# Kernel tuning notes

Hardware: AMD Instinct MI355X
Metric: run time of the kernel (lower is better)

The kernel has to match this reference:

```python
import jax, jax.numpy as jnp
import numpy as np

NQ = 10000   # num_q
N = 512      # n (seq len)
D = 512      # d (model dim)
H = 8        # attention heads
LW = 64      # local window
B = 16       # batch


def _mha(q, k, v, wi, bi, wo, bo, nh, mask=None):
    # torch nn.MultiheadAttention math (eval mode, dropout off), batch-first inputs
    Bq, S, d = q.shape
    hd = d // nh
    wq, wk, wv = jnp.split(wi, 3, axis=0)
    bq, bk, bv = jnp.split(bi, 3)

    def proj(x, w, b):
        y = x @ w.T + b
        return y.reshape(x.shape[0], x.shape[1], nh, hd).transpose(0, 2, 1, 3)  # [B,h,S,hd]

    Q = proj(q, wq, bq)
    K = proj(k, wk, bk)
    V = proj(v, wv, bv)
    s = jnp.einsum('bhqe,bhke->bhqk', Q, K) / jnp.sqrt(jnp.asarray(hd, q.dtype))
    if mask is not None:
        s = jnp.where(mask[None, None], -jnp.inf, s)
    w = jax.nn.softmax(s, axis=-1)
    o = jnp.einsum('bhqk,bhke->bhqe', w, V).transpose(0, 2, 1, 3).reshape(Bq, S, d)
    return o @ wo.T + bo, w.mean(axis=1)  # avg over heads like torch default


def _ln(x, g, b):
    m = x.mean(-1, keepdims=True)
    v = ((x - m) ** 2).mean(-1, keepdims=True)
    return (x - m) / jnp.sqrt(v + 1e-5) * g + b


def setup_inputs() -> dict:
    key = jax.random.key(0)
    ks = iter(jax.random.split(key, 40))
    f = lambda *sh: jax.random.normal(next(ks), sh, jnp.float32) * 0.02
    inp = {
        'q': jax.random.randint(next(ks), (B, N), 0, NQ, jnp.int32),
        'r': jax.random.randint(next(ks), (B, N), 0, 2, jnp.int32),
        'qry': jax.random.randint(next(ks), (B, N), 0, NQ, jnp.int32),
        'M_emb': f(2 * NQ, D),
        'E_emb': f(NQ, D),
        'P': f(N, D),
    }
    for nm in ['base', 'local', 'glob', 'cross']:
        inp[nm + '_in_w'] = f(3 * D, D)
        inp[nm + '_in_b'] = jnp.zeros((3 * D,), jnp.float32)
        inp[nm + '_out_w'] = f(D, D)
        inp[nm + '_out_b'] = jnp.zeros((D,), jnp.float32)
    inp['ln1_g'] = jnp.ones((D,), jnp.float32)
    inp['ln1_b'] = jnp.zeros((D,), jnp.float32)
    inp['w1'] = f(D, D)
    inp['b1'] = jnp.zeros((D,), jnp.float32)
    inp['w2'] = f(D, D)
    inp['b2'] = jnp.zeros((D,), jnp.float32)
    inp['ln2_g'] = jnp.ones((D,), jnp.float32)
    inp['ln2_b'] = jnp.zeros((D,), jnp.float32)
    inp['pred_w'] = f(1, D)
    inp['pred_b'] = jnp.zeros((1,), jnp.float32)
    return inp


def reference(q, r, qry, M_emb, E_emb, P,
              base_in_w, base_in_b, base_out_w, base_out_b,
              local_in_w, local_in_b, local_out_w, local_out_b,
              glob_in_w, glob_in_b, glob_out_w, glob_out_b,
              cross_in_w, cross_in_b, cross_out_w, cross_out_b,
              ln1_g, ln1_b, w1, b1, w2, b2, ln2_g, ln2_b, pred_w, pred_b):
    x = q + NQ * r
    M = M_emb[x] + P[None]          # [B,N,D], positional added as in torch code
    E = E_emb[qry]                  # [B,N,D]
    cm = jnp.triu(jnp.ones((N, N), bool), 1)

    S_base, attn_w = _mha(E, M, M, base_in_w, base_in_b, base_out_w, base_out_b, H, cm)
    S_base = _ln(S_base + M + E, ln1_g, ln1_b)

    lm = jnp.triu(jnp.ones((LW, LW), bool), 1)
    s_loc_in = S_base[:, -LW:, :]
    S_loc, _ = _mha(s_loc_in, s_loc_in, s_loc_in, local_in_w, local_in_b, local_out_w, local_out_b, H, lm)
    S_local = jnp.concatenate([jnp.zeros((S_base.shape[0], N - LW, D), S_base.dtype), S_loc], axis=1)

    S_global, _ = _mha(S_base, S_base, S_base, glob_in_w, glob_in_b, glob_out_w, glob_out_b, H, cm)
    S_cross, _ = _mha(S_base, S_local, S_local, cross_in_w, cross_in_b, cross_out_w, cross_out_b, H, None)

    S = S_base + S_local + S_global + S_cross
    F = jax.nn.relu(S @ w1.T + b1) @ w2.T + b2
    F = _ln(F + S, ln2_g, ln2_b)
    p = jax.nn.sigmoid(F @ pred_w.T + pred_b)[..., 0]   # [B,N]
    return p, attn_w
```

## Files before the change

kernel.cpp:

```cpp
#include <hip/hip_runtime.h>
#include <hip/hip_bf16.h>

#define D_MODEL 512
#define NHEAD 8
#define NSEQ 512
#define BATCH 16
#define LWIN 64
#define S2C 0.18033688f
#define L2E 1.44269504f

typedef short s16x8 __attribute__((ext_vector_type(8)));
typedef float f32x4 __attribute__((ext_vector_type(4)));

__device__ inline unsigned short f2bf(float f) {
    unsigned int u = __float_as_uint(f);
    u = (u + 0x7fffu + ((u >> 16) & 1u)) >> 16;
    return (unsigned short)u;
}
__device__ inline int sw4(int r) { return (r + (r >> 2)) & 3; }

#define GLD16(g, l) __builtin_amdgcn_global_load_lds( \
    (const __attribute__((address_space(1))) void*)(g), \
    (__attribute__((address_space(3))) void*)(l), 16, 0, 0)

struct WP { const float* p[10]; };

__global__ __launch_bounds__(256) void front_kernel(
    WP wp, unsigned short* __restrict__ Wb, unsigned short* __restrict__ Z,
    const int* __restrict__ q, const int* __restrict__ r, const int* __restrict__ qry,
    const float* __restrict__ M_emb, const float* __restrict__ E_emb,
    const float* __restrict__ P, float* __restrict__ Mf, float* __restrict__ Ef,
    unsigned short* __restrict__ Mb, unsigned short* __restrict__ Eb)
{
    const int blk = blockIdx.x, tid = threadIdx.x;
    if (blk < 4608) {
        const long e = ((long)blk * 256 + tid) * 4;
        const float* src; long loc;
        if (e < 3145728) { int rg = (int)(e / 786432); src = wp.p[rg]; loc = e - (long)rg * 786432; }
        else { long j = e - 3145728; int rg = (int)(j >> 18); src = wp.p[4 + rg]; loc = j - ((long)rg << 18); }
        float4 v = *(const float4*)(src + loc);
        ushort4 o; o.x = f2bf(v.x); o.y = f2bf(v.y); o.z = f2bf(v.z); o.w = f2bf(v.w);
        *(ushort4*)(Wb + e) = o;
    } else if (blk < 6656) {
        const long i = ((long)(blk - 4608) * 256 + tid) * 8;
        *(uint4*)(Z + i) = make_uint4(0u, 0u, 0u, 0u);
    } else {
        const int t = (blk - 6656) * 2 + (tid >> 7);
        const int i = tid & 127;
        const int n = t & (NSEQ - 1);
        const int x = q[t] + 10000 * r[t];
        const int e = qry[t];
        float4 a = ((const float4*)(M_emb + (long)x * D_MODEL))[i];
        float4 p4 = ((const float4*)(P + (long)n * D_MODEL))[i];
        float4 ev = ((const float4*)(E_emb + (long)e * D_MODEL))[i];
        float4 mv = make_float4(a.x + p4.x, a.y + p4.y, a.z + p4.z, a.w + p4.w);
        ((float4*)(Mf + (long)t * D_MODEL))[i] = mv;
        ((float4*)(Ef + (long)t * D_MODEL))[i] = ev;
        ushort4 mb; mb.x = f2bf(mv.x); mb.y = f2bf(mv.y); mb.z = f2bf(mv.z); mb.w = f2bf(mv.w);
        ushort4 eb; eb.x = f2bf(ev.x); eb.y = f2bf(ev.y); eb.z = f2bf(ev.z); eb.w = f2bf(ev.w);
        *(ushort4*)(Mb + (long)t * D_MODEL + i * 4) = mb;
        *(ushort4*)(Eb + (long)t * D_MODEL + i * 4) = eb;
    }
}

struct GArgs {
    const unsigned short* A; const unsigned short* A2; int nsplit;
    const unsigned short* W; const float* bias;
    unsigned short* Cb; int ldcb; int crem;
    float* Cf; int ldcf;
    const float* r1; const float* r2; const float* tl;
    int relu; int arem;
};

__global__ __launch_bounds__(256) void gemm_bf16(GArgs g0, GArgs g1, int msplit)
{
    __shared__ __align__(16) unsigned short Sh[6144];
    unsigned short* As = Sh;
    unsigned short* Ws = Sh + 4096;
    float* Shf = (float*)Sh;

    int m0 = blockIdx.y * 128;
    const GArgs& G = (m0 < msplit) ? g0 : g1;
    if (m0 >= msplit) m0 -= msplit;

    const int tid = threadIdx.x, lane = tid & 63, wid = tid >> 6;
    const int n0 = blockIdx.x * 64;
    const int lm = lane & 15;
    const int lq = lane >> 4;
    const unsigned short* Asel = (n0 >= G.nsplit) ? G.A2 : G.A;

    const int rlane = lane >> 2, clane = lane & 3;
    const int lr0 = wid * 16 + rlane;
    const int lr1 = 64 + lr0;
    int rgA0 = m0 + lr0, rgA1 = m0 + lr1;
    if (G.arem) {
        rgA0 = ((rgA0 >> 6) << 9) + (NSEQ - LWIN) + (rgA0 & 63);
        rgA1 = ((rgA1 >> 6) << 9) + (NSEQ - LWIN) + (rgA1 & 63);
    }
    const unsigned short* pA0 = Asel + (long)rgA0 * 512 + ((clane ^ sw4(lr0)) << 3);
    const unsigned short* pA1 = Asel + (long)rgA1 * 512 + ((clane ^ sw4(lr1)) << 3);
    const unsigned short* pW0 = G.W + (long)(n0 + lr0) * 512 + ((clane ^ sw4(lr0)) << 3);
    unsigned short* lA0 = As + (wid * 16) * 32;
    unsigned short* lA1 = As + (64 + wid * 16) * 32;
    unsigned short* lW0 = Ws + (wid * 16) * 32;

    f32x4 acc[2][4];
    #pragma unroll
    for (int i = 0; i < 2; ++i)
        #pragma unroll
        for (int j = 0; j < 4; ++j) acc[i][j] = (f32x4){0.f, 0.f, 0.f, 0.f};

    for (int k0 = 0; k0 < 512; k0 += 32) {
        __syncthreads();
        GLD16(pA0 + k0, lA0);
        GLD16(pA1 + k0, lA1);
        GLD16(pW0 + k0, lW0);
        __syncthreads();

        s16x8 af[2], wf[4];
        #pragma unroll
        for (int i = 0; i < 2; ++i) {
            const int ra = wid * 32 + i * 16 + lm;
            af[i] = *(const s16x8*)&As[ra * 32 + ((lq ^ sw4(ra)) << 3)];
        }
        #pragma unroll
        for (int j = 0; j < 4; ++j) {
            const int rw = j * 16 + lm;
            wf[j] = *(const s16x8*)&Ws[rw * 32 + ((lq ^ sw4(rw)) << 3)];
        }
        #pragma unroll
        for (int i = 0; i < 2; ++i)
            #pragma unroll
            for (int j = 0; j < 4; ++j)
                acc[i][j] = __builtin_amdgcn_mfma_f32_16x16x32_bf16(af[i], wf[j], acc[i][j], 0, 0, 0);
    }

    const int fr = lane & 15;
    const int q4 = (lane >> 4) * 4;
    for (int qtr = 0; qtr < 4; ++qtr) {
        __syncthreads();
        if (wid == qtr) {
            #pragma unroll
            for (int j = 0; j < 4; ++j) {
                const int lcol = j * 16 + fr;
                const float bv = G.bias[n0 + lcol];
                #pragma unroll
                for (int i = 0; i < 2; ++i) {
                    #pragma unroll
                    for (int rg = 0; rg < 4; ++rg) {
                        float v = acc[i][j][rg] + bv;
                        if (G.relu) v = fmaxf(v, 0.f);
                        Shf[(i * 16 + q4 + rg) * 68 + lcol] = v;
                    }
                }
            }
        }
        __syncthreads();
        #pragma unroll
        for (int it = 0; it < 2; ++it) {
            const int flat = it * 256 + tid;
            const int rowq = flat >> 4, k4 = flat & 15;
            const int grow = m0 + qtr * 32 + rowq;
            const int gcol = n0 + k4 * 4;
            float4 f = *(const float4*)&Shf[rowq * 68 + k4 * 4];
            if (G.r1) {
                float4 a = *(const float4*)(G.r1 + (long)grow * 512 + gcol);
                f.x += a.x; f.y += a.y; f.z += a.z; f.w += a.w;
            }
            if (G.r2) {
                float4 b = *(const float4*)(G.r2 + (long)grow * 512 + gcol);
                f.x += b.x; f.y += b.y; f.z += b.z; f.w += b.w;
            }
            if (G.tl) {
                const int n = grow & 511;
                if (n >= NSEQ - LWIN) {
                    float4 c = *(const float4*)(G.tl + ((long)(grow >> 9) * 64 + (n - (NSEQ - LWIN))) * 512 + gcol);
                    f.x += c.x; f.y += c.y; f.z += c.z; f.w += c.w;
                }
            }
            if (G.Cf) *(float4*)(G.Cf + (long)grow * G.ldcf + gcol) = f;
            if (G.Cb) {
                const int crow = G.crem ? (((grow >> 6) << 9) + (NSEQ - LWIN) + (grow & 63)) : grow;
                ushort4 u; u.x = f2bf(f.x); u.y = f2bf(f.y); u.z = f2bf(f.z); u.w = f2bf(f.w);
                *(ushort4*)(G.Cb + (long)crow * G.ldcb + gcol) = u;
            }
        }
    }
}

struct FArgs {
    const unsigned short* Q; const unsigned short* K; const unsigned short* V;
    unsigned short* O; float* stats; int Nq, Nkv, ldq, ldkv, causal;
};

__global__ __launch_bounds__(256) void flash_mfma(FArgs f0, FArgs f1, int xsplit)
{
    __shared__ __align__(16) unsigned short Ks[64 * 72];
    __shared__ __align__(16) unsigned short Pl[64 * 72];
    __shared__ __align__(16) unsigned int   Vt[64 * 36];

    const FArgs& F = ((int)blockIdx.x < xsplit) ? f0 : f1;
    const int bx = ((int)blockIdx.x < xsplit) ? blockIdx.x : (blockIdx.x - xsplit);

    const int tid = threadIdx.x, lane = tid & 63, w = tid >> 6;
    const int lm = lane & 15, lq = lane >> 4;
    const int h = blockIdx.y, b = blockIdx.z;
    const int Nq = F.Nq, Nkv = F.Nkv, ldq = F.ldq, ldkv = F.ldkv, causal = F.causal;
    const int nqt = Nq >> 6;
    const int qa = bx, qb = nqt - 1 - qa;
    const bool single = (qa == qb);

    s16x8 aqA0, aqA1, aqB0, aqB1;
    {
        const unsigned short* qp = F.Q + ((long)b * Nq + qb * 64 + w * 16 + lm) * ldq + h * 64 + lq * 8;
        aqB0 = *(const s16x8*)qp; aqB1 = *(const s16x8*)(qp + 32);
    }
    if (!single) {
        const unsigned short* qp = F.Q + ((long)b * Nq + qa * 64 + w * 16 + lm) * ldq + h * 64 + lq * 8;
        aqA0 = *(const s16x8*)qp; aqA1 = *(const s16x8*)(qp + 32);
    }

    float mA = -INFINITY, lA = 0.f, mB = -INFINITY, lB = 0.f;
    f32x4 oA[4], oB[4];
    #pragma unroll
    for (int t = 0; t < 4; ++t) { oA[t] = (f32x4){0.f,0.f,0.f,0.f}; oB[t] = (f32x4){0.f,0.f,0.f,0.f}; }

    const int nkt = causal ? (qb + 1) : (Nkv >> 6);
    const int skey = tid >> 3, sd = (tid & 7) * 8;

    s16x8 kr0, kr1; uint4 vr0, vr1;
    {
        const long kb = ((long)b * Nkv) * ldkv + h * 64;
        kr0 = *(const s16x8*)(F.K + kb + (long)skey * ldkv + sd);
        kr1 = *(const s16x8*)(F.K + kb + (long)(skey + 32) * ldkv + sd);
        const unsigned short* vp = F.V + ((long)b * Nkv + 2 * skey) * ldkv + h * 64 + sd;
        vr0 = *(const uint4*)vp; vr1 = *(const uint4*)(vp + ldkv);
    }

    auto process = [&](s16x8 a0, s16x8 a1, float& m, float& l, f32x4* oacc, bool diag) {
        f32x4 sc[4];
        #pragma unroll
        for (int t = 0; t < 4; ++t) sc[t] = (f32x4){0.f,0.f,0.f,0.f};
        #pragma unroll
        for (int t = 0; t < 4; ++t) {
            s16x8 k0 = *(const s16x8*)&Ks[(t * 16 + lm) * 72 + lq * 8];
            s16x8 k1 = *(const s16x8*)&Ks[(t * 16 + lm) * 72 + lq * 8 + 32];
            sc[t] = __builtin_amdgcn_mfma_f32_16x16x32_bf16(k0, a0, sc[t], 0, 0, 0);
            sc[t] = __builtin_amdgcn_mfma_f32_16x16x32_bf16(k1, a1, sc[t], 0, 0, 0);
        }
        if (diag) {
            #pragma unroll
            for (int t = 0; t < 4; ++t)
                #pragma unroll
                for (int r = 0; r < 4; ++r)
                    if (t * 16 + lq * 4 + r > w * 16 + lm) sc[t][r] = -INFINITY;
        }
        float mt = sc[0][0];
        #pragma unroll
        for (int t = 0; t < 4; ++t)
            #pragma unroll
            for (int r = 0; r < 4; ++r) mt = fmaxf(mt, sc[t][r]);
        mt = fmaxf(mt, __shfl_xor(mt, 16));
        mt = fmaxf(mt, __shfl_xor(mt, 32));
        const float mn = fmaxf(m, mt);
        const float al = exp2f((m - mn) * S2C);
        float rs = 0.f;
        #pragma unroll
        for (int t = 0; t < 4; ++t)
            #pragma unroll
            for (int r = 0; r < 4; ++r) {
                float p = exp2f((sc[t][r] - mn) * S2C);
                sc[t][r] = p; rs += p;
            }
        rs += __shfl_xor(rs, 16);
        rs += __shfl_xor(rs, 32);
        m = mn; l = l * al + rs;
        #pragma unroll
        for (int t = 0; t < 4; ++t) oacc[t] *= al;
        #pragma unroll
        for (int t = 0; t < 4; ++t) {
            ushort4 u;
            u.x = f2bf(sc[t][0]); u.y = f2bf(sc[t][1]);
            u.z = f2bf(sc[t][2]); u.w = f2bf(sc[t][3]);
            *(ushort4*)&Pl[(w * 16 + lm) * 72 + t * 16 + lq * 4] = u;
        }
        #pragma unroll
        for (int ks = 0; ks < 2; ++ks) {
            s16x8 bp = *(const s16x8*)&Pl[(w * 16 + lm) * 72 + ks * 32 + lq * 8];
            #pragma unroll
            for (int t = 0; t < 4; ++t) {
                const int row = t * 16 + lm;
                const int pg = ((lq >> 1) + 2 * ks) ^ ((row >> 3) & 3);
                s16x8 av = *(const s16x8*)((const unsigned short*)Vt + row * 72 + pg * 16 + (lq & 1) * 8);
                oacc[t] = __builtin_amdgcn_mfma_f32_16x16x32_bf16(av, bp, oacc[t], 0, 0, 0);
            }
        }
    };

    for (int kt = 0; kt < nkt; ++kt) {
        __syncthreads();
        *(s16x8*)&Ks[skey * 72 + sd] = kr0;
        *(s16x8*)&Ks[(skey + 32) * 72 + sd] = kr1;
        {
            unsigned pw[8];
            pw[0] = (vr0.x & 0xffffu) | (vr1.x << 16);
            pw[1] = (vr0.x >> 16)     | (vr1.x & 0xffff0000u);
            pw[2] = (vr0.y & 0xffffu) | (vr1.y << 16);
            pw[3] = (vr0.y >> 16)     | (vr1.y & 0xffff0000u);
            pw[4] = (vr0.z & 0xffffu) | (vr1.z << 16);
            pw[5] = (vr0.z >> 16)     | (vr1.z & 0xffff0000u);
            pw[6] = (vr0.w & 0xffffu) | (vr1.w << 16);
            pw[7] = (vr0.w >> 16)     | (vr1.w & 0xffff0000u);
            #pragma unroll
            for (int j = 0; j < 8; ++j) {
                const int row = sd + j;
                const int col = (((skey >> 3) ^ ((row >> 3) & 3)) << 3) | (skey & 7);
                Vt[row * 36 + col] = pw[j];
            }
        }
        __syncthreads();
        if (kt + 1 < nkt) {
            const long kb = ((long)b * Nkv + (kt + 1) * 64) * ldkv + h * 64;
            kr0 = *(const s16x8*)(F.K + kb + (long)skey * ldkv + sd);
            kr1 = *(const s16x8*)(F.K + kb + (long)(skey + 32) * ldkv + sd);
            const unsigned short* vp = F.V + ((long)b * Nkv + (kt + 1) * 64 + 2 * skey) * ldkv + h * 64 + sd;
            vr0 = *(const uint4*)vp; vr1 = *(const uint4*)(vp + ldkv);
        }
        process(aqB0, aqB1, mB, lB, oB, causal && (kt == qb));
        if (!single && (!causal || kt <= qa))
            process(aqA0, aqA1, mA, lA, oA, causal && (kt == qa));
    }

    {
        const float inv = 1.0f / lB;
        const long orow = ((long)b * Nq + qb * 64 + w * 16 + lm) * D_MODEL + h * 64;
        #pragma unroll
        for (int t = 0; t < 4; ++t) {
            ushort4 u;
            u.x = f2bf(oB[t][0] * inv); u.y = f2bf(oB[t][1] * inv);
            u.z = f2bf(oB[t][2] * inv); u.w = f2bf(oB[t][3] * inv);
            *(ushort4*)(F.O + orow + t * 16 + lq * 4) = u;
        }
    }
    if (!single) {
        const float inv = 1.0f / lA;
        const long orow = ((long)b * Nq + qa * 64 + w * 16 + lm) * D_MODEL + h * 64;
        #pragma unroll
        for (int t = 0; t < 4; ++t) {
            ushort4 u;
            u.x = f2bf(oA[t][0] * inv); u.y = f2bf(oA[t][1] * inv);
            u.z = f2bf(oA[t][2] * inv); u.w = f2bf(oA[t][3] * inv);
            *(ushort4*)(F.O + orow + t * 16 + lq * 4) = u;
        }
    }
    if (F.stats && lq == 0) {
        long idx = (((long)b * NHEAD + h) * Nq + qb * 64 + w * 16 + lm) * 2;
        F.stats[idx] = mB * 0.125f; F.stats[idx + 1] = lB;
        if (!single) {
            idx = (((long)b * NHEAD + h) * Nq + qa * 64 + w * 16 + lm) * 2;
            F.stats[idx] = mA * 0.125f; F.stats[idx + 1] = lA;
        }
    }
}

__global__ __launch_bounds__(256) void attn_w_kernel(
    const unsigned short* __restrict__ Q, const unsigned short* __restrict__ K,
    const float* __restrict__ stats, float* __restrict__ AW, int ldq, int ldk)
{
    const int kt = blockIdx.x, qt = blockIdx.y, b = blockIdx.z;
    const int tid = threadIdx.x;
    if (kt > qt) {
        const int tx = tid & 15, ty = tid >> 4;
        #pragma unroll
        for (int i = 0; i < 4; ++i)
            *(float4*)(AW + ((long)b * NSEQ + qt * 64 + ty * 4 + i) * NSEQ + kt * 64 + tx * 4)
                = make_float4(0.f, 0.f, 0.f, 0.f);
        return;
    }
    __shared__ __align__(16) unsigned short Ks[64 * 72];
    const int lane = tid & 63, w = tid >> 6;
    const int lm = lane & 15, lq = lane >> 4;
    const int skey = tid >> 3, sd = (tid & 7) * 8;
    const long qrow = (long)b * NSEQ + qt * 64 + w * 16 + lm;

    f32x4 aw[4];
    #pragma unroll
    for (int t = 0; t < 4; ++t) aw[t] = (f32x4){0.f,0.f,0.f,0.f};

    for (int h = 0; h < NHEAD; ++h) {
        __syncthreads();
        {
            const long kb = ((long)b * NSEQ + kt * 64) * ldk + h * 64;
            *(s16x8*)&Ks[skey * 72 + sd] = *(const s16x8*)(K + kb + (long)skey * ldk + sd);
            *(s16x8*)&Ks[(skey + 32) * 72 + sd] = *(const s16x8*)(K + kb + (long)(skey + 32) * ldk + sd);
        }
        __syncthreads();
        s16x8 a0, a1;
        {
            const unsigned short* qp = Q + qrow * ldq + h * 64 + lq * 8;
            a0 = *(const s16x8*)qp; a1 = *(const s16x8*)(qp + 32);
        }
        f32x4 sc[4];
        #pragma unroll
        for (int t = 0; t < 4; ++t) sc[t] = (f32x4){0.f,0.f,0.f,0.f};
        #pragma unroll
        for (int t = 0; t < 4; ++t) {
            s16x8 k0 = *(const s16x8*)&Ks[(t * 16 + lm) * 72 + lq * 8];
            s16x8 k1 = *(const s16x8*)&Ks[(t * 16 + lm) * 72 + lq * 8 + 32];
            sc[t] = __builtin_amdgcn_mfma_f32_16x16x32_bf16(k0, a0, sc[t], 0, 0, 0);
            sc[t] = __builtin_amdgcn_mfma_f32_16x16x32_bf16(k1, a1, sc[t], 0, 0, 0);
        }
        float2 ml = *(const float2*)(stats + (((long)b * NHEAD + h) * NSEQ + qt * 64 + w * 16 + lm) * 2);
        const float mb2 = ml.x * L2E;
        const float sca = 0.125f / ml.y;
        #pragma unroll
        for (int t = 0; t < 4; ++t)
            #pragma unroll
            for (int r = 0; r < 4; ++r) {
                const bool masked = (kt == qt) && (t * 16 + lq * 4 + r > w * 16 + lm);
                if (!masked) aw[t][r] += exp2f(sc[t][r] * S2C - mb2) * sca;
            }
    }
    #pragma unroll
    for (int t = 0; t < 4; ++t)
        *(float4*)(AW + qrow * NSEQ + kt * 64 + t * 16 + lq * 4) = float4{aw[t][0], aw[t][1], aw[t][2], aw[t][3]};
}

__global__ __launch_bounds__(256) void ln_kernel(
    const float* __restrict__ X, const float* __restrict__ R1,
    const float* __restrict__ R2, const float* __restrict__ g,
    const float* __restrict__ bb, float* __restrict__ outf,
    unsigned short* __restrict__ outb,
    const float* __restrict__ pw, const float* __restrict__ pb,
    float* __restrict__ outp)
{
    const long row = blockIdx.x;
    const int tid = threadIdx.x;
    __shared__ float red[256];
    const long base = row * D_MODEL;
    float v0 = X[base + tid], v1 = X[base + tid + 256];
    if (R1) { v0 += R1[base + tid]; v1 += R1[base + tid + 256]; }
    if (R2) { v0 += R2[base + tid]; v1 += R2[base + tid + 256]; }
    red[tid] = v0 + v1; __syncthreads();
    for (int s = 128; s > 0; s >>= 1) {
        if (tid < s) red[tid] += red[tid + s];
        __syncthreads();
    }
    const float mean = red[0] * (1.f / 512.f);
    __syncthreads();
    const float d0 = v0 - mean, d1 = v1 - mean;
    red[tid] = d0 * d0 + d1 * d1; __syncthreads();
    for (int s = 128; s > 0; s >>= 1) {
        if (tid < s) red[tid] += red[tid + s];
        __syncthreads();
    }
    const float rstd = rsqrtf(red[0] * (1.f / 512.f) + 1e-5f);
    const float y0 = d0 * rstd * g[tid] + bb[tid];
    const float y1 = d1 * rstd * g[tid + 256] + bb[tid + 256];
    if (pw) {
        float s = y0 * pw[tid] + y1 * pw[tid + 256];
        __syncthreads();
        red[tid] = s; __syncthreads();
        for (int st = 128; st > 0; st >>= 1) {
            if (tid < st) red[tid] += red[tid + st];
            __syncthreads();
        }
        if (tid == 0) outp[row] = 1.f / (1.f + __expf(-(red[0] + pb[0])));
        return;
    }
    if (outf) { outf[base + tid] = y0; outf[base + tid + 256] = y1; }
    if (outb) { outb[base + tid] = f2bf(y0); outb[base + tid + 256] = f2bf(y1); }
}

extern "C" void kernel_launch(void* const* d_in, const int* in_sizes, int n_in,
                              void* d_out, int out_size, void* d_ws, size_t ws_size,
                              hipStream_t stream)
{
    const int*   q          = (const int*)d_in[0];
    const int*   r          = (const int*)d_in[1];
    const int*   qry        = (const int*)d_in[2];
    const float* M_emb      = (const float*)d_in[3];
    const float* E_emb      = (const float*)d_in[4];
    const float* P          = (const float*)d_in[5];
    const float* base_in_w  = (const float*)d_in[6];
    const float* base_in_b  = (const float*)d_in[7];
    const float* base_out_w = (const float*)d_in[8];
    const float* base_out_b = (const float*)d_in[9];
    const float* local_in_w = (const float*)d_in[10];
    const float* local_in_b = (const float*)d_in[11];
    const float* local_out_w= (const float*)d_in[12];
    const float* local_out_b= (const float*)d_in[13];
    const float* glob_in_w  = (const float*)d_in[14];
    const float* glob_in_b  = (const float*)d_in[15];
    const float* glob_out_w = (const float*)d_in[16];
    const float* glob_out_b = (const float*)d_in[17];
    const float* cross_in_w = (const float*)d_in[18];
    const float* cross_in_b = (const float*)d_in[19];
    const float* cross_out_w= (const float*)d_in[20];
    const float* cross_out_b= (const float*)d_in[21];
    const float* ln1_g      = (const float*)d_in[22];
    const float* ln1_b      = (const float*)d_in[23];
    const float* w1         = (const float*)d_in[24];
    const float* b1         = (const float*)d_in[25];
    const float* w2         = (const float*)d_in[26];
    const float* b2         = (const float*)d_in[27];
    const float* ln2_g      = (const float*)d_in[28];
    const float* ln2_b      = (const float*)d_in[29];
    const float* pred_w     = (const float*)d_in[30];
    const float* pred_b     = (const float*)d_in[31];
    float* out = (float*)d_out;

    char* p = (char*)d_ws;
    unsigned short* Wb = (unsigned short*)p; p += 4718592L * 2;
    unsigned short* B[11];
    for (int i = 0; i < 11; ++i) { B[i] = (unsigned short*)p; p += 8388608L; }
    unsigned short* Obl   = (unsigned short*)p; p += 1048576L;
    unsigned short* QKV3L = (unsigned short*)p; p += 3145728L;
    float* R[4];
    for (int i = 0; i < 4; ++i) { R[i] = (float*)p; p += 16777216L; }
    float* Tloc  = (float*)p; p += 2097152L;
    float* stats = (float*)p; p += 524288L;

    unsigned short* Mb = B[0];
    unsigned short* Eb = B[1];      unsigned short* Oc_b = B[1];
    unsigned short* QKVb = B[2];
    unsigned short* Sb_b = B[2];
    unsigned short* Ob  = B[5];
    unsigned short* Sbase_b  = B[6];
    unsigned short* Slocal_b = B[7];
    unsigned short* QKV3 = B[8];
    unsigned short* H1_b = B[8];
    float* Mf = R[0];
    float* Ef = R[1];       float* Sbuf_f   = R[1];
    float* Tb_f = R[2];     float* Sglobal_f= R[2];
    float* Sbase_f = R[3];  float* Fpre_f   = R[3];

    const long oBin = 0, oLin = 786432, oGin = 1572864, oCin = 2359296;
    const long oBout = 3145728, oLout = 3407872, oGout = 3670016, oCout = 3932160;
    const long oW1 = 4194304, oW2 = 4456448;
    const int BIG = 1 << 30;
    const unsigned short* NUS = nullptr;
    const float* NF = nullptr;

    auto GA = [](const unsigned short* A, const unsigned short* A2, int nsplit,
                 const unsigned short* W, const float* bias,
                 unsigned short* Cb, int ldcb, int crem, float* Cf, int ldcf,
                 const float* r1, const float* r2, const float* tl, int relu, int arem) {
        GArgs g; g.A = A; g.A2 = A2; g.nsplit = nsplit; g.W = W; g.bias = bias;
        g.Cb = Cb; g.ldcb = ldcb; g.crem = crem; g.Cf = Cf; g.ldcf = ldcf;
        g.r1 = r1; g.r2 = r2; g.tl = tl; g.relu = relu; g.arem = arem; return g;
    };
    auto FA = [](const unsigned short* Q, const unsigned short* K, const unsigned short* V,
                 unsigned short* O, float* stats, int Nq, int Nkv, int ldq, int ldkv, int causal) {
        FArgs f; f.Q = Q; f.K = K; f.V = V; f.O = O; f.stats = stats;
        f.Nq = Nq; f.Nkv = Nkv; f.ldq = ldq; f.ldkv = ldkv; f.causal = causal; return f;
    };

    WP wp; wp.p[0] = base_in_w; wp.p[1] = local_in_w; wp.p[2] = glob_in_w; wp.p[3] = cross_in_w;
    wp.p[4] = base_out_w; wp.p[5] = local_out_w; wp.p[6] = glob_out_w; wp.p[7] = cross_out_w;
    wp.p[8] = w1; wp.p[9] = w2;
    front_kernel<<<10752, 256, 0, stream>>>(wp, Wb, Slocal_b, q, r, qry, M_emb, E_emb, P, Mf, Ef, Mb, Eb);

    GArgs gBase = GA(Eb, Mb, 512, Wb + oBin, base_in_b, QKVb, 1536, 0, nullptr, 0, NF, NF, NF, 0, 0);
    gemm_bf16<<<dim3(24, 64), 256, 0, stream>>>(gBase, gBase, BIG);
    FArgs fBase = FA(QKVb, QKVb + 512, QKVb + 1024, Ob, stats, 512, 512, 1536, 1536, 1);
    flash_mfma<<<dim3(4, NHEAD, BATCH), 256, 0, stream>>>(fBase, fBase, BIG);
    attn_w_kernel<<<dim3(8, 8, BATCH), 256, 0, stream>>>(QKVb, QKVb + 512, stats, out + 8192, 1536, 1536);
    GArgs gBo = GA(Ob, NUS, BIG, Wb + oBout, base_out_b, nullptr, 0, 0, Tb_f, 512, Mf, Ef, NF, 0, 0);
    gemm_bf16<<<dim3(8, 64), 256, 0, stream>>>(gBo, gBo, BIG);
    ln_kernel<<<8192, 256, 0, stream>>>(Tb_f, NF, NF, ln1_g, ln1_b, Sbase_f, Sbase_b, NF, NF, nullptr);

    GArgs gGin = GA(Sbase_b, NUS, BIG, Wb + oGin, glob_in_b, QKV3, 1536, 0, nullptr, 0, NF, NF, NF, 0, 0);
    GArgs gLin = GA(Sbase_b, NUS, BIG, Wb + oLin, local_in_b, QKV3L, 1536, 0, nullptr, 0, NF, NF, NF, 0, 1);
    gemm_bf16<<<dim3(24, 72), 256, 0, stream>>>(gGin, gLin, 8192);

    FArgs fGlob = FA(QKV3, QKV3 + 512, QKV3 + 1024, Ob, nullptr, 512, 512, 1536, 1536, 1);
    FArgs fLoc  = FA(QKV3L, QKV3L + 512, QKV3L + 1024, Obl, nullptr, 64, 64, 1536, 1536, 1);
    flash_mfma<<<dim3(5, NHEAD, BATCH), 256, 0, stream>>>(fGlob, fLoc, 4);

    GArgs gGo = GA(Ob, NUS, BIG, Wb + oGout, glob_out_b, nullptr, 0, 0, Sglobal_f, 512, NF, NF, NF, 0, 0);
    GArgs gLo = GA(Obl, NUS, BIG, Wb + oLout, local_out_b, Slocal_b, 512, 1, Tloc, 512, NF, NF, NF, 0, 0);
    gemm_bf16<<<dim3(8, 72), 256, 0, stream>>>(gGo, gLo, 8192);

    GArgs gCin = GA(Sbase_b, Slocal_b, 512, Wb + oCin, cross_in_b, QKVb, 1536, 0, nullptr, 0, NF, NF, NF, 0, 0);
    gemm_bf16<<<dim3(24, 64), 256, 0, stream>>>(gCin, gCin, BIG);
    FArgs fCross = FA(QKVb, QKVb + 512, QKVb + 1024, Oc_b, nullptr, 512, 512, 1536, 1536, 0);
    flash_mfma<<<dim3(4, NHEAD, BATCH), 256, 0, stream>>>(fCross, fCross, BIG);
    GArgs gCo = GA(Oc_b, NUS, BIG, Wb + oCout, cross_out_b, Sb_b, 512, 0, Sbuf_f, 512,
                   Sbase_f, Sglobal_f, Tloc, 0, 0);
    gemm_bf16<<<dim3(8, 64), 256, 0, stream>>>(gCo, gCo, BIG);

    GArgs gF1 = GA(Sb_b, NUS, BIG, Wb + oW1, b1, H1_b, 512, 0, nullptr, 0, NF, NF, NF, 1, 0);
    gemm_bf16<<<dim3(8, 64), 256, 0, stream>>>(gF1, gF1, BIG);
    GArgs gF2 = GA(H1_b, NUS, BIG, Wb + oW2, b2, nullptr, 0, 0, Fpre_f, 512, Sbuf_f, NF, NF, 0, 0);
    gemm_bf16<<<dim3(8, 64), 256, 0, stream>>>(gF2, gF2, BIG);
    ln_kernel<<<8192, 256, 0, stream>>>(Fpre_f, NF, NF, ln2_g, ln2_b,
        nullptr, nullptr, pred_w, pred_b, out);
}
```

Before: 497.0 us.

## Store fp32 intermediates as bf16 and fuse attention-weight kernel into QKV GEMM launch

Every fp32 intermediate (embeddings, residual sums, pre-LN outputs, global/local branches) is now stored and read as bf16, which removes the fp32 copies and roughly halves the memory traffic of the epilogues and layernorms. The standalone attention-weight kernel is merged into the global/local QKV GEMM launch as extra blocks, so the two run concurrently and one launch is saved. The cost is lower precision on the residual paths and layernorm inputs, which could move outputs closer to the tolerance limit.

```diff
diff --git a/kernel.cpp b/kernel.cpp
--- a/kernel.cpp
+++ b/kernel.cpp
@@ -17,6 +17,11 @@
     u = (u + 0x7fffu + ((u >> 16) & 1u)) >> 16;
     return (unsigned short)u;
 }
+__device__ inline float4 bfl4(const unsigned short* p) {
+    uint2 u = *(const uint2*)p;
+    return make_float4(__uint_as_float(u.x << 16), __uint_as_float(u.x & 0xffff0000u),
+                       __uint_as_float(u.y << 16), __uint_as_float(u.y & 0xffff0000u));
+}
 __device__ inline int sw4(int r) { return (r + (r >> 2)) & 3; }
 
 #define GLD16(g, l) __builtin_amdgcn_global_load_lds( \
@@ -29,7 +34,7 @@
     WP wp, unsigned short* __restrict__ Wb, unsigned short* __restrict__ Z,
     const int* __restrict__ q, const int* __restrict__ r, const int* __restrict__ qry,
     const float* __restrict__ M_emb, const float* __restrict__ E_emb,
-    const float* __restrict__ P, float* __restrict__ Mf, float* __restrict__ Ef,
+    const float* __restrict__ P,
     unsigned short* __restrict__ Mb, unsigned short* __restrict__ Eb)
 {
     const int blk = blockIdx.x, tid = threadIdx.x;
@@ -54,8 +59,6 @@
         float4 p4 = ((const float4*)(P + (long)n * D_MODEL))[i];
         float4 ev = ((const float4*)(E_emb + (long)e * D_MODEL))[i];
         float4 mv = make_float4(a.x + p4.x, a.y + p4.y, a.z + p4.z, a.w + p4.w);
-        ((float4*)(Mf + (long)t * D_MODEL))[i] = mv;
-        ((float4*)(Ef + (long)t * D_MODEL))[i] = ev;
         ushort4 mb; mb.x = f2bf(mv.x); mb.y = f2bf(mv.y); mb.z = f2bf(mv.z); mb.w = f2bf(mv.w);
         ushort4 eb; eb.x = f2bf(ev.x); eb.y = f2bf(ev.y); eb.z = f2bf(ev.z); eb.w = f2bf(ev.w);
         *(ushort4*)(Mb + (long)t * D_MODEL + i * 4) = mb;
@@ -67,24 +70,19 @@
     const unsigned short* A; const unsigned short* A2; int nsplit;
     const unsigned short* W; const float* bias;
     unsigned short* Cb; int ldcb; int crem;
-    float* Cf; int ldcf;
-    const float* r1; const float* r2; const float* tl;
+    unsigned short* Cb2; int ldcb2;
+    const unsigned short* r1; const unsigned short* r2; const unsigned short* tl;
     int relu; int arem;
 };
 
-__global__ __launch_bounds__(256) void gemm_bf16(GArgs g0, GArgs g1, int msplit)
-{
-    __shared__ __align__(16) unsigned short Sh[6144];
+__device__ __forceinline__ void gemm_body(unsigned short* Sh, const GArgs& G,
+                                          int n0, int m0, int tid)
+{
     unsigned short* As = Sh;
     unsigned short* Ws = Sh + 4096;
     float* Shf = (float*)Sh;
 
-    int m0 = blockIdx.y * 128;
-    const GArgs& G = (m0 < msplit) ? g0 : g1;
-    if (m0 >= msplit) m0 -= msplit;
-
-    const int tid = threadIdx.x, lane = tid & 63, wid = tid >> 6;
-    const int n0 = blockIdx.x * 64;
+    const int lane = tid & 63, wid = tid >> 6;
     const int lm = lane & 15;
     const int lq = lane >> 4;
     const unsigned short* Asel = (n0 >= G.nsplit) ? G.A2 : G.A;
@@ -164,27 +162,114 @@
             const int gcol = n0 + k4 * 4;
             float4 f = *(const float4*)&Shf[rowq * 68 + k4 * 4];
             if (G.r1) {
-                float4 a = *(const float4*)(G.r1 + (long)grow * 512 + gcol);
+                float4 a = bfl4(G.r1 + (long)grow * 512 + gcol);
                 f.x += a.x; f.y += a.y; f.z += a.z; f.w += a.w;
             }
             if (G.r2) {
-                float4 b = *(const float4*)(G.r2 + (long)grow * 512 + gcol);
+                float4 b = bfl4(G.r2 + (long)grow * 512 + gcol);
                 f.x += b.x; f.y += b.y; f.z += b.z; f.w += b.w;
             }
             if (G.tl) {
                 const int n = grow & 511;
                 if (n >= NSEQ - LWIN) {
-                    float4 c = *(const float4*)(G.tl + ((long)(grow >> 9) * 64 + (n - (NSEQ - LWIN))) * 512 + gcol);
+                    float4 c = bfl4(G.tl + ((long)(grow >> 9) * 64 + (n - (NSEQ - LWIN))) * 512 + gcol);
                     f.x += c.x; f.y += c.y; f.z += c.z; f.w += c.w;
                 }
             }
-            if (G.Cf) *(float4*)(G.Cf + (long)grow * G.ldcf + gcol) = f;
+            ushort4 u; u.x = f2bf(f.x); u.y = f2bf(f.y); u.z = f2bf(f.z); u.w = f2bf(f.w);
             if (G.Cb) {
                 const int crow = G.crem ? (((grow >> 6) << 9) + (NSEQ - LWIN) + (grow & 63)) : grow;
-                ushort4 u; u.x = f2bf(f.x); u.y = f2bf(f.y); u.z = f2bf(f.z); u.w = f2bf(f.w);
                 *(ushort4*)(G.Cb + (long)crow * G.ldcb + gcol) = u;
             }
-        }
+            if (G.Cb2) *(ushort4*)(G.Cb2 + (long)grow * G.ldcb2 + gcol) = u;
+        }
+    }
+}
+
+__global__ __launch_bounds__(256) void gemm_bf16(GArgs g0, GArgs g1, int msplit)
+{
+    __shared__ __align__(16) unsigned short Sh[6144];
+    int m0 = blockIdx.y * 128;
+    const GArgs& G = (m0 < msplit) ? g0 : g1;
+    if (m0 >= msplit) m0 -= msplit;
+    gemm_body(Sh, G, blockIdx.x * 64, m0, threadIdx.x);
+}
+
+__device__ __forceinline__ void attnw_body(unsigned short* Ks,
+    const unsigned short* __restrict__ Q, const unsigned short* __restrict__ K,
+    const float* __restrict__ stats, float* __restrict__ AW, int ldq, int ldk,
+    int kt, int qt, int b, int tid)
+{
+    if (kt > qt) {
+        const int tx = tid & 15, ty = tid >> 4;
+        #pragma unroll
+        for (int i = 0; i < 4; ++i)
+            *(float4*)(AW + ((long)b * NSEQ + qt * 64 + ty * 4 + i) * NSEQ + kt * 64 + tx * 4)
+                = make_float4(0.f, 0.f, 0.f, 0.f);
+        return;
+    }
+    const int lane = tid & 63, w = tid >> 6;
+    const int lm = lane & 15, lq = lane >> 4;
+    const int skey = tid >> 3, sd = (tid & 7) * 8;
+    const long qrow = (long)b * NSEQ + qt * 64 + w * 16 + lm;
+
+    f32x4 aw[4];
+    #pragma unroll
+    for (int t = 0; t < 4; ++t) aw[t] = (f32x4){0.f,0.f,0.f,0.f};
+
+    for (int h = 0; h < NHEAD; ++h) {
+        __syncthreads();
+        {
+            const long kb = ((long)b * NSEQ + kt * 64) * ldk + h * 64;
+            *(s16x8*)&Ks[skey * 72 + sd] = *(const s16x8*)(K + kb + (long)skey * ldk + sd);
+            *(s16x8*)&Ks[(skey + 32) * 72 + sd] = *(const s16x8*)(K + kb + (long)(skey + 32) * ldk + sd);
+        }
+        __syncthreads();
+        s16x8 a0, a1;
+        {
+            const unsigned short* qp = Q + qrow * ldq + h * 64 + lq * 8;
+            a0 = *(const s16x8*)qp; a1 = *(const s16x8*)(qp + 32);
+        }
+        f32x4 sc[4];
+        #pragma unroll
+        for (int t = 0; t < 4; ++t) sc[t] = (f32x4){0.f,0.f,0.f,0.f};
+        #pragma unroll
+        for (int t = 0; t < 4; ++t) {
+            s16x8 k0 = *(const s16x8*)&Ks[(t * 16 + lm) * 72 + lq * 8];
+            s16x8 k1 = *(const s16x8*)&Ks[(t * 16 + lm) * 72 + lq * 8 + 32];
+            sc[t] = __builtin_amdgcn_mfma_f32_16x16x32_bf16(k0, a0, sc[t], 0, 0, 0);
+            sc[t] = __builtin_amdgcn_mfma_f32_16x16x32_bf16(k1, a1, sc[t], 0, 0, 0);
+        }
+        float2 ml = *(const float2*)(stats + (((long)b * NHEAD + h) * NSEQ + qt * 64 + w * 16 + lm) * 2);
+        const float mb2 = ml.x * L2E;
+        const float sca = 0.125f / ml.y;
+        #pragma unroll
+        for (int t = 0; t < 4; ++t)
+            #pragma unroll
+            for (int r = 0; r < 4; ++r) {
+                const bool masked = (kt == qt) && (t * 16 + lq * 4 + r > w * 16 + lm);
+                if (!masked) aw[t][r] += exp2f(sc[t][r] * S2C - mb2) * sca;
+            }
+    }
+    #pragma unroll
+    for (int t = 0; t < 4; ++t)
+        *(float4*)(AW + qrow * NSEQ + kt * 64 + t * 16 + lq * 4) = float4{aw[t][0], aw[t][1], aw[t][2], aw[t][3]};
+}
+
+__global__ __launch_bounds__(256) void gemm_attnw(GArgs g0, GArgs g1, int msplit,
+    const unsigned short* Q, const unsigned short* K, const float* stats,
+    float* AW, int ldq, int ldk)
+{
+    __shared__ __align__(16) unsigned short Sh[6144];
+    const int x = blockIdx.x;
+    if (x < 1728) {
+        int m0 = (x / 24) * 128;
+        const GArgs& G = (m0 < msplit) ? g0 : g1;
+        if (m0 >= msplit) m0 -= msplit;
+        gemm_body(Sh, G, (x % 24) * 64, m0, threadIdx.x);
+    } else {
+        const int id = x - 1728;
+        attnw_body(Sh, Q, K, stats, AW, ldq, ldk, id & 7, (id >> 3) & 7, id >> 6, threadIdx.x);
     }
 }
 
@@ -363,74 +448,9 @@
     }
 }
 
-__global__ __launch_bounds__(256) void attn_w_kernel(
-    const unsigned short* __restrict__ Q, const unsigned short* __restrict__ K,
-    const float* __restrict__ stats, float* __restrict__ AW, int ldq, int ldk)
-{
-    const int kt = blockIdx.x, qt = blockIdx.y, b = blockIdx.z;
-    const int tid = threadIdx.x;
-    if (kt > qt) {
-        const int tx = tid & 15, ty = tid >> 4;
-        #pragma unroll
-        for (int i = 0; i < 4; ++i)
-            *(float4*)(AW + ((long)b * NSEQ + qt * 64 + ty * 4 + i) * NSEQ + kt * 64 + tx * 4)
-                = make_float4(0.f, 0.f, 0.f, 0.f);
-        return;
-    }
-    __shared__ __align__(16) unsigned short Ks[64 * 72];
-    const int lane = tid & 63, w = tid >> 6;
-    const int lm = lane & 15, lq = lane >> 4;
-    const int skey = tid >> 3, sd = (tid & 7) * 8;
-    const long qrow = (long)b * NSEQ + qt * 64 + w * 16 + lm;
-
-    f32x4 aw[4];
-    #pragma unroll
-    for (int t = 0; t < 4; ++t) aw[t] = (f32x4){0.f,0.f,0.f,0.f};
-
-    for (int h = 0; h < NHEAD; ++h) {
-        __syncthreads();
-        {
-            const long kb = ((long)b * NSEQ + kt * 64) * ldk + h * 64;
-            *(s16x8*)&Ks[skey * 72 + sd] = *(const s16x8*)(K + kb + (long)skey * ldk + sd);
-            *(s16x8*)&Ks[(skey + 32) * 72 + sd] = *(const s16x8*)(K + kb + (long)(skey + 32) * ldk + sd);
-        }
-        __syncthreads();
-        s16x8 a0, a1;
-        {
-            const unsigned short* qp = Q + qrow * ldq + h * 64 + lq * 8;
-            a0 = *(const s16x8*)qp; a1 = *(const s16x8*)(qp + 32);
-        }
-        f32x4 sc[4];
-        #pragma unroll
-        for (int t = 0; t < 4; ++t) sc[t] = (f32x4){0.f,0.f,0.f,0.f};
-        #pragma unroll
-        for (int t = 0; t < 4; ++t) {
-            s16x8 k0 = *(const s16x8*)&Ks[(t * 16 + lm) * 72 + lq * 8];
-            s16x8 k1 = *(const s16x8*)&Ks[(t * 16 + lm) * 72 + lq * 8 + 32];
-            sc[t] = __builtin_amdgcn_mfma_f32_16x16x32_bf16(k0, a0, sc[t], 0, 0, 0);
-            sc[t] = __builtin_amdgcn_mfma_f32_16x16x32_bf16(k1, a1, sc[t], 0, 0, 0);
-        }
-        float2 ml = *(const float2*)(stats + (((long)b * NHEAD + h) * NSEQ + qt * 64 + w * 16 + lm) * 2);
-        const float mb2 = ml.x * L2E;
-        const float sca = 0.125f / ml.y;
-        #pragma unroll
-        for (int t = 0; t < 4; ++t)
-            #pragma unroll
-            for (int r = 0; r < 4; ++r) {
-                const bool masked = (kt == qt) && (t * 16 + lq * 4 + r > w * 16 + lm);
-                if (!masked) aw[t][r] += exp2f(sc[t][r] * S2C - mb2) * sca;
-            }
-    }
-    #pragma unroll
-    for (int t = 0; t < 4; ++t)
-        *(float4*)(AW + qrow * NSEQ + kt * 64 + t * 16 + lq * 4) = float4{aw[t][0], aw[t][1], aw[t][2], aw[t][3]};
-}
-
 __global__ __launch_bounds__(256) void ln_kernel(
-    const float* __restrict__ X, const float* __restrict__ R1,
-    const float* __restrict__ R2, const float* __restrict__ g,
-    const float* __restrict__ bb, float* __restrict__ outf,
-    unsigned short* __restrict__ outb,
+    const unsigned short* __restrict__ X, const float* __restrict__ g,
+    const float* __restrict__ bb, unsigned short* __restrict__ outb,
     const float* __restrict__ pw, const float* __restrict__ pb,
     float* __restrict__ outp)
 {
@@ -438,9 +458,9 @@
     const int tid = threadIdx.x;
     __shared__ float red[256];
     const long base = row * D_MODEL;
-    float v0 = X[base + tid], v1 = X[base + tid + 256];
-    if (R1) { v0 += R1[base + tid]; v1 += R1[base + tid + 256]; }
-    if (R2) { v0 += R2[base + tid]; v1 += R2[base + tid + 256]; }
+    const unsigned ux = *(const unsigned*)(X + base + tid * 2);
+    const float v0 = __uint_as_float(ux << 16);
+    const float v1 = __uint_as_float(ux & 0xffff0000u);
     red[tid] = v0 + v1; __syncthreads();
     for (int s = 128; s > 0; s >>= 1) {
         if (tid < s) red[tid] += red[tid + s];
@@ -455,10 +475,13 @@
         __syncthreads();
     }
     const float rstd = rsqrtf(red[0] * (1.f / 512.f) + 1e-5f);
-    const float y0 = d0 * rstd * g[tid] + bb[tid];
-    const float y1 = d1 * rstd * g[tid + 256] + bb[tid + 256];
+    const float2 gv = *(const float2*)(g + tid * 2);
+    const float2 bv = *(const float2*)(bb + tid * 2);
+    const float y0 = d0 * rstd * gv.x + bv.x;
+    const float y1 = d1 * rstd * gv.y + bv.y;
     if (pw) {
-        float s = y0 * pw[tid] + y1 * pw[tid + 256];
+        const float2 pv = *(const float2*)(pw + tid * 2);
+        float s = y0 * pv.x + y1 * pv.y;
         __syncthreads();
         red[tid] = s; __syncthreads();
         for (int st = 128; st > 0; st >>= 1) {
@@ -468,8 +491,8 @@
         if (tid == 0) outp[row] = 1.f / (1.f + __expf(-(red[0] + pb[0])));
         return;
     }
-    if (outf) { outf[base + tid] = y0; outf[base + tid + 256] = y1; }
-    if (outb) { outb[base + tid] = f2bf(y0); outb[base + tid + 256] = f2bf(y1); }
+    const unsigned o = (unsigned)f2bf(y0) | ((unsigned)f2bf(y1) << 16);
+    *(unsigned*)(outb + base + tid * 2) = o;
 }
 
 extern "C" void kernel_launch(void* const* d_in, const int* in_sizes, int n_in,
@@ -514,11 +537,12 @@
     unsigned short* Wb = (unsigned short*)p; p += 4718592L * 2;
     unsigned short* B[11];
     for (int i = 0; i < 11; ++i) { B[i] = (unsigned short*)p; p += 8388608L; }
-    unsigned short* Obl   = (unsigned short*)p; p += 1048576L;
-    unsigned short* QKV3L = (unsigned short*)p; p += 3145728L;
-    float* R[4];
-    for (int i = 0; i < 4; ++i) { R[i] = (float*)p; p += 16777216L; }
-    float* Tloc  = (float*)p; p += 2097152L;
+    unsigned short* Obl    = (unsigned short*)p; p += 1048576L;
+    unsigned short* QKV3L  = (unsigned short*)p; p += 3145728L;
+    unsigned short* Tb_b   = (unsigned short*)p; p += 8388608L;
+    unsigned short* Sglobal_b = (unsigned short*)p; p += 8388608L;
+    unsigned short* Fpre_b = (unsigned short*)p; p += 8388608L;
+    unsigned short* Tloc_b = (unsigned short*)p; p += 1048576L;
     float* stats = (float*)p; p += 524288L;
 
     unsigned short* Mb = B[0];
@@ -530,10 +554,6 @@
     unsigned short* Slocal_b = B[7];
     unsigned short* QKV3 = B[8];
     unsigned short* H1_b = B[8];
-    float* Mf = R[0];
-    float* Ef = R[1];       float* Sbuf_f   = R[1];
-    float* Tb_f = R[2];     float* Sglobal_f= R[2];
-    float* Sbase_f = R[3];  float* Fpre_f   = R[3];
 
     const long oBin = 0, oLin = 786432, oGin = 1572864, oCin = 2359296;
     const long oBout = 3145728, oLout = 3407872, oGout = 3670016, oCout = 3932160;
@@ -544,10 +564,12 @@
 
     auto GA = [](const unsigned short* A, const unsigned short* A2, int nsplit,
                  const unsigned short* W, const float* bias,
-                 unsigned short* Cb, int ldcb, int crem, float* Cf, int ldcf,
-                 const float* r1, const float* r2, const float* tl, int relu, int arem) {
+                 unsigned short* Cb, int ldcb, int crem,
+                 unsigned short* Cb2, int ldcb2,
+                 const unsigned short* r1, const unsigned short* r2,
+                 const unsigned short* tl, int relu, int arem) {
         GArgs g; g.A = A; g.A2 = A2; g.nsplit = nsplit; g.W = W; g.bias = bias;
-        g.Cb = Cb; g.ldcb = ldcb; g.crem = crem; g.Cf = Cf; g.ldcf = ldcf;
+        g.Cb = Cb; g.ldcb = ldcb; g.crem = crem; g.Cb2 = Cb2; g.ldcb2 = ldcb2;
         g.r1 = r1; g.r2 = r2; g.tl = tl; g.relu = relu; g.arem = arem; return g;
     };
     auto FA = [](const unsigned short* Q, const unsigned short* K, const unsigned short* V,
@@ -559,41 +581,39 @@
     WP wp; wp.p[0] = base_in_w; wp.p[1] = local_in_w; wp.p[2] = glob_in_w; wp.p[3] = cross_in_w;
     wp.p[4] = base_out_w; wp.p[5] = local_out_w; wp.p[6] = glob_out_w; wp.p[7] = cross_out_w;
     wp.p[8] = w1; wp.p[9] = w2;
-    front_kernel<<<10752, 256, 0, stream>>>(wp, Wb, Slocal_b, q, r, qry, M_emb, E_emb, P, Mf, Ef, Mb, Eb);
-
-    GArgs gBase = GA(Eb, Mb, 512, Wb + oBin, base_in_b, QKVb, 1536, 0, nullptr, 0, NF, NF, NF, 0, 0);
+    front_kernel<<<10752, 256, 0, stream>>>(wp, Wb, Slocal_b, q, r, qry, M_emb, E_emb, P, Mb, Eb);
+
+    GArgs gBase = GA(Eb, Mb, 512, Wb + oBin, base_in_b, QKVb, 1536, 0, nullptr, 0, NUS, NUS, NUS, 0, 0);
     gemm_bf16<<<dim3(24, 64), 256, 0, stream>>>(gBase, gBase, BIG);
     FArgs fBase = FA(QKVb, QKVb + 512, QKVb + 1024, Ob, stats, 512, 512, 1536, 1536, 1);
     flash_mfma<<<dim3(4, NHEAD, BATCH), 256, 0, stream>>>(fBase, fBase, BIG);
-    attn_w_kernel<<<dim3(8, 8, BATCH), 256, 0, stream>>>(QKVb, QKVb + 512, stats, out + 8192, 1536, 1536);
-    GArgs gBo = GA(Ob, NUS, BIG, Wb + oBout, base_out_b, nullptr, 0, 0, Tb_f, 512, Mf, Ef, NF, 0, 0);
+    GArgs gBo = GA(Ob, NUS, BIG, Wb + oBout, base_out_b, Tb_b, 512, 0, nullptr, 0, Mb, Eb, NUS, 0, 0);
     gemm_bf16<<<dim3(8, 64), 256, 0, stream>>>(gBo, gBo, BIG);
-    ln_kernel<<<8192, 256, 0, stream>>>(Tb_f, NF, NF, ln1_g, ln1_b, Sbase_f, Sbase_b, NF, NF, nullptr);
-
-    GArgs gGin = GA(Sbase_b, NUS, BIG, Wb + oGin, glob_in_b, QKV3, 1536, 0, nullptr, 0, NF, NF, NF, 0, 0);
-    GArgs gLin = GA(Sbase_b, NUS, BIG, Wb + oLin, local_in_b, QKV3L, 1536, 0, nullptr, 0, NF, NF, NF, 0, 1);
-    gemm_bf16<<<dim3(24, 72), 256, 0, stream>>>(gGin, gLin, 8192);
+    ln_kernel<<<8192, 256, 0, stream>>>(Tb_b, ln1_g, ln1_b, Sbase_b, NF, NF, nullptr);
+
+    GArgs gGin = GA(Sbase_b, NUS, BIG, Wb + oGin, glob_in_b, QKV3, 1536, 0, nullptr, 0, NUS, NUS, NUS, 0, 0);
+    GArgs gLin = GA(Sbase_b, NUS, BIG, Wb + oLin, local_in_b, QKV3L, 1536, 0, nullptr, 0, NUS, NUS, NUS, 0, 1);
+    gemm_attnw<<<2752, 256, 0, stream>>>(gGin, gLin, 8192, QKVb, QKVb + 512, stats, out + 8192, 1536, 1536);
 
     FArgs fGlob = FA(QKV3, QKV3 + 512, QKV3 + 1024, Ob, nullptr, 512, 512, 1536, 1536, 1);
     FArgs fLoc  = FA(QKV3L, QKV3L + 512, QKV3L + 1024, Obl, nullptr, 64, 64, 1536, 1536, 1);
     flash_mfma<<<dim3(5, NHEAD, BATCH), 256, 0, stream>>>(fGlob, fLoc, 4);
 
-    GArgs gGo = GA(Ob, NUS, BIG, Wb + oGout, glob_out_b, nullptr, 0, 0, Sglobal_f, 512, NF, NF, NF, 0, 0);
-    GArgs gLo = GA(Obl, NUS, BIG, Wb + oLout, local_out_b, Slocal_b, 512, 1, Tloc, 512, NF, NF, NF, 0, 0);
+    GArgs gGo = GA(Ob, NUS, BIG, Wb + oGout, glob_out_b, Sglobal_b, 512, 0, nullptr, 0, NUS, NUS, NUS, 0, 0);
+    GArgs gLo = GA(Obl, NUS, BIG, Wb + oLout, local_out_b, Slocal_b, 512, 1, Tloc_b, 512, NUS, NUS, NUS, 0, 0);
     gemm_bf16<<<dim3(8, 72), 256, 0, stream>>>(gGo, gLo, 8192);
 
-    GArgs gCin = GA(Sbase_b, Slocal_b, 512, Wb + oCin, cross_in_b, QKVb, 1536, 0, nullptr, 0, NF, NF, NF, 0, 0);
+    GArgs gCin = GA(Sbase_b, Slocal_b, 512, Wb + oCin, cross_in_b, QKVb, 1536, 0, nullptr, 0, NUS, NUS, NUS, 0, 0);
     gemm_bf16<<<dim3(24, 64), 256, 0, stream>>>(gCin, gCin, BIG);
     FArgs fCross = FA(QKVb, QKVb + 512, QKVb + 1024, Oc_b, nullptr, 512, 512, 1536, 1536, 0);
     flash_mfma<<<dim3(4, NHEAD, BATCH), 256, 0, stream>>>(fCross, fCross, BIG);
-    GArgs gCo = GA(Oc_b, NUS, BIG, Wb + oCout, cross_out_b, Sb_b, 512, 0, Sbuf_f, 512,
-                   Sbase_f, Sglobal_f, Tloc, 0, 0);
+    GArgs gCo = GA(Oc_b, NUS, BIG, Wb + oCout, cross_out_b, Sb_b, 512, 0, nullptr, 0,
+                   Sbase_b, Sglobal_b, Tloc_b, 0, 0);
     gemm_bf16<<<dim3(8, 64), 256, 0, stream>>>(gCo, gCo, BIG);
 
-    GArgs gF1 = GA(Sb_b, NUS, BIG, Wb + oW1, b1, H1_b, 512, 0, nullptr, 0, NF, NF, NF, 1, 0);
+    GArgs gF1 = GA(Sb_b, NUS, BIG, Wb + oW1, b1, H1_b, 512, 0, nullptr, 0, NUS, NUS, NUS, 1, 0);
     gemm_bf16<<<dim3(8, 64), 256, 0, stream>>>(gF1, gF1, BIG);
-    GArgs gF2 = GA(H1_b, NUS, BIG, Wb + oW2, b2, nullptr, 0, 0, Fpre_f, 512, Sbuf_f, NF, NF, 0, 0);
+    GArgs gF2 = GA(H1_b, NUS, BIG, Wb + oW2, b2, Fpre_b, 512, 0, nullptr, 0, Sb_b, NUS, NUS, 0, 0);
     gemm_bf16<<<dim3(8, 64), 256, 0, stream>>>(gF2, gF2, BIG);
-    ln_kernel<<<8192, 256, 0, stream>>>(Fpre_f, NF, NF, ln2_g, ln2_b,
-        nullptr, nullptr, pred_w, pred_b, out);
-}
+    ln_kernel<<<8192, 256, 0, stream>>>(Fpre_b, ln2_g, ln2_b, nullptr, pred_w, pred_b, out);
+}
```

After: 644.5 us. +29.7%, slower.
